# Performance work log

Hardware: AMD Instinct MI355X
Metric: run time of the kernel (lower is better)

The kernel has to match this reference:

```python
import jax, jax.numpy as jnp
import numpy as np

N_NODES = 100_000
N_EDGES = 3_200_000
D_FEAT = 128
L_FILTERS = 10  # filter_count_L
ALPHA = 0.3


def setup_inputs() -> dict:
    key = jax.random.key(0)
    k1, k2, k3, k4 = jax.random.split(key, 4)
    edge_row = jax.random.randint(k1, (N_EDGES,), 0, N_NODES, dtype=jnp.int32)
    edge_col = jax.random.randint(k2, (N_EDGES,), 0, N_NODES, dtype=jnp.int32)
    # scale ~1/avg_degree so the propagated signal stays well-conditioned over 10 hops
    edge_vals = jax.random.uniform(k3, (N_EDGES,), dtype=jnp.float32) * (1.0 / 32.0)
    X = jax.random.normal(k4, (N_NODES, D_FEAT), dtype=jnp.float32)
    # reset_parameters: gpr_weights[i] = alpha * (1-alpha)**i
    gpr_weights = ALPHA * (1.0 - ALPHA) ** jnp.arange(L_FILTERS + 1, dtype=jnp.float32)
    return {"edge_row": edge_row, "edge_col": edge_col, "edge_vals": edge_vals,
            "X": X, "gpr_weights": gpr_weights}


def reference(edge_row, edge_col, edge_vals, X, gpr_weights):
    """GPR filter bank: Z = sum_l w_l * A^l X (dropout is identity at inference)."""
    n = X.shape[0]
    H = X                                  # hop 0
    out = gpr_weights[0] * X
    for l in range(1, L_FILTERS + 1):
        msgs = edge_vals[:, None] * H[edge_col]          # [E, d] gather + scale
        H = jax.ops.segment_sum(msgs, edge_row, num_segments=n)  # SpMM row-scatter
        H = jnp.where(jnp.isfinite(H), H, jnp.zeros_like(H))     # non-finite guard
        out = out + gpr_weights[l] * H
    return out
```

## Files before the change

### kernel.cpp

```cpp
#include <hip/hip_runtime.h>
#include <math.h>

#define N_NODES   100000
#define D_FEAT    128
#define N_EDGES   3200000
#define L_FILTERS 10

#define RPB_LOG   7
#define RPB       128
#define NBUCKETS  ((N_NODES + RPB - 1) >> RPB_LOG)
#define CHUNK     8192
#define NA_BLOCKS ((N_EDGES + CHUNK - 1) / CHUNK)

typedef unsigned char  u8;
typedef unsigned int   u32;
typedef unsigned short u16;
typedef unsigned long long u64;
typedef float f32x2 __attribute__((ext_vector_type(2)));

static __device__ __forceinline__ u16 f2bf(float f) {
    u32 u = __float_as_uint(f);
    u32 r = (u + 0x7FFFu + ((u >> 16) & 1u)) >> 16;
    return (u16)r;
}
static __device__ __forceinline__ float bf2f(u32 b) {
    return __uint_as_float(b << 16);
}

__global__ void gpr_init(const float* __restrict__ X,
                         u16* __restrict__ Xbf, u8* __restrict__ Xf8, int n4) {
    int i = blockIdx.x * blockDim.x + threadIdx.x;
    if (i >= n4) return;
    float4 v = ((const float4*)X)[i];
    ushort4 b;
    b.x = f2bf(v.x); b.y = f2bf(v.y); b.z = f2bf(v.z); b.w = f2bf(v.w);
    ((ushort4*)Xbf)[i] = b;
    u32 p01 = __builtin_amdgcn_cvt_pk_fp8_f32(v.x, v.y, 0, false) & 0xFFFFu;
    u32 p23 = __builtin_amdgcn_cvt_pk_fp8_f32(v.z, v.w, 0, false) & 0xFFFFu;
    ((u32*)Xf8)[i] = p01 | (p23 << 16);
}

__global__ __launch_bounds__(256) void gpr_bucket_hist(const int* __restrict__ rows,
                                                       int* __restrict__ bcount) {
    __shared__ int hist[NBUCKETS];
    int t = threadIdx.x;
    for (int i = t; i < NBUCKETS; i += 256) hist[i] = 0;
    __syncthreads();
    int stride = gridDim.x * 256;
    for (int e = blockIdx.x * 256 + t; e < N_EDGES; e += stride)
        atomicAdd(&hist[rows[e] >> RPB_LOG], 1);
    __syncthreads();
    for (int i = t; i < NBUCKETS; i += 256)
        if (hist[i]) atomicAdd(&bcount[i], hist[i]);
}

__global__ __launch_bounds__(1024) void gpr_bucket_scan(const int* __restrict__ bcount,
                                                        int* __restrict__ bucket_base,
                                                        int* __restrict__ bucket_cursor,
                                                        int* __restrict__ row_ptr) {
    __shared__ int buf[1024];
    int t = threadIdx.x;
    int v = (t < NBUCKETS) ? bcount[t] : 0;
    buf[t] = v; __syncthreads();
    for (int off = 1; off < 1024; off <<= 1) {
        int x = (t >= off) ? buf[t - off] : 0;
        __syncthreads();
        buf[t] += x;
        __syncthreads();
    }
    if (t < NBUCKETS) {
        int ex = buf[t] - v;
        bucket_base[t] = ex;
        bucket_cursor[t] = ex;
    }
    if (t == 0) {
        bucket_base[NBUCKETS] = N_EDGES;
        row_ptr[N_NODES] = N_EDGES;
    }
}

__global__ __launch_bounds__(256) void gpr_binA(const int* __restrict__ rows,
                                                const int* __restrict__ cols,
                                                const float* __restrict__ vals,
                                                int* __restrict__ bucket_cursor,
                                                u64* __restrict__ packedA) {
    __shared__ u64 stage[CHUNK];
    __shared__ int hist[NBUCKETS];
    __shared__ int lbase[NBUCKETS];
    __shared__ int lcur[NBUCKETS];
    __shared__ int goff[NBUCKETS];
    __shared__ int psum[256];
    int t = threadIdx.x;
    long long base = (long long)blockIdx.x * CHUNK;
    for (int i = t; i < NBUCKETS; i += 256) hist[i] = 0;
    __syncthreads();
    for (int j = 0; j < CHUNK / 256; ++j) {
        long long e = base + j * 256 + t;
        if (e < N_EDGES) atomicAdd(&hist[rows[e] >> RPB_LOG], 1);
    }
    __syncthreads();
    int s = 0, b0 = t * 4;
    #pragma unroll
    for (int j = 0; j < 4; ++j) { int b = b0 + j; if (b < NBUCKETS) s += hist[b]; }
    psum[t] = s; __syncthreads();
    for (int off = 1; off < 256; off <<= 1) {
        int x = (t >= off) ? psum[t - off] : 0;
        __syncthreads();
        psum[t] += x;
        __syncthreads();
    }
    int run = psum[t] - s;
    #pragma unroll
    for (int j = 0; j < 4; ++j) {
        int b = b0 + j;
        if (b < NBUCKETS) { lbase[b] = run; run += hist[b]; }
    }
    __syncthreads();
    for (int i = t; i < NBUCKETS; i += 256) {
        lcur[i] = lbase[i];
        int g = (hist[i]) ? atomicAdd(&bucket_cursor[i], hist[i]) : 0;
        goff[i] = g - lbase[i];
    }
    __syncthreads();
    for (int j = 0; j < CHUNK / 256; ++j) {
        long long e = base + j * 256 + t;
        if (e < N_EDGES) {
            int r = rows[e];
            u32 vb = (u32)f2bf(vals[e]);
            u64 p = ((u64)vb << 34) | ((u64)(u32)r << 17) | (u64)(u32)cols[e];
            int pos = atomicAdd(&lcur[r >> RPB_LOG], 1);
            stage[pos] = p;
        }
    }
    __syncthreads();
    long long rem = (long long)N_EDGES - base;
    int total = (rem < CHUNK) ? (int)rem : CHUNK;
    for (int idx = t; idx < total; idx += 256) {
        u64 p = stage[idx];
        int b = (int)((p >> 17) & 0x1FFFFu) >> RPB_LOG;
        packedA[goff[b] + idx] = p;
    }
}

__global__ __launch_bounds__(256) void gpr_binB(const int* __restrict__ bucket_base,
                                                const u64* __restrict__ packedA,
                                                int* __restrict__ row_ptr,
                                                u32* __restrict__ edges) {
    __shared__ int cnt[RPB];
    __shared__ int sbuf[RPB];
    __shared__ int cur[RPB];
    int b = blockIdx.x;
    int t = threadIdx.x;
    int r0 = b << RPB_LOG;
    int r1 = r0 + RPB; if (r1 > N_NODES) r1 = N_NODES;
    int lo = bucket_base[b], hi = bucket_base[b + 1];
    if (t < RPB) cnt[t] = 0;
    __syncthreads();
    for (int e = lo + t; e < hi; e += 256) {
        int r = (int)((packedA[e] >> 17) & 0x1FFFFu);
        atomicAdd(&cnt[r - r0], 1);
    }
    __syncthreads();
    if (t < RPB) sbuf[t] = cnt[t];
    __syncthreads();
    for (int off = 1; off < RPB; off <<= 1) {
        int x = (t < RPB && t >= off) ? sbuf[t - off] : 0;
        __syncthreads();
        if (t < RPB) sbuf[t] += x;
        __syncthreads();
    }
    if (t < RPB) {
        int ex = sbuf[t] - cnt[t];
        cur[t] = ex;
        if (r0 + t < r1) row_ptr[r0 + t] = lo + ex;
    }
    __syncthreads();
    for (int e = lo + t; e < hi; e += 256) {
        u64 p = packedA[e];
        int r = (int)((p >> 17) & 0x1FFFFu);
        int pos = lo + atomicAdd(&cur[r - r0], 1);
        edges[pos] = (u32)(((p >> 34) << 17) | (p & 0x1FFFFu));
    }
}


#define IS8(EW, TT, H)                                                          \
    { _Pragma("unroll")                                                         \
      for (int j = 0; j < 8; ++j) {                                             \
          u32 es = (u32)__builtin_amdgcn_readlane((int)(EW), (TT) + j);         \
          H[j] = *(const u16*)((const u8*)H8 + (size_t)((es & 0x1FFFFu) << 7) + lane2); \
      } }

#define CO8(EW, M, TT, H, PX, PY)                                               \
    { _Pragma("unroll")                                                         \
      for (int j = 0; j < 8; ++j) {                                             \
          int t = (TT) + j;                                                     \
          u32 es = (u32)__builtin_amdgcn_readlane((int)(EW), t);                \
          float v = (t < (M)) ? __uint_as_float((es >> 17) << 16) : 0.0f;       \
          f32x2 f = __builtin_amdgcn_cvt_pk_f32_fp8(H[j], false);               \
          PX[j & 3] = fmaf(v, f[0], PX[j & 3]);                                 \
          PY[j & 3] = fmaf(v, f[1], PY[j & 3]);                                 \
      } }

#define PIPE(EW, M, PX, PY)                                                     \
    {                                                                           \
        u32 hA[8], hB[8];                                                       \
        IS8(EW, 0, hA)                                                          \
        if ((M) > 8)  IS8(EW, 8, hB)                                            \
        CO8(EW, M, 0, hA, PX, PY)                                               \
        if ((M) > 16) IS8(EW, 16, hA)                                           \
        if ((M) > 8)  CO8(EW, M, 8, hB, PX, PY)                                 \
        if ((M) > 24) IS8(EW, 24, hB)                                           \
        if ((M) > 16) CO8(EW, M, 16, hA, PX, PY)                                \
        if ((M) > 32) IS8(EW, 32, hA)                                           \
        if ((M) > 24) CO8(EW, M, 24, hB, PX, PY)                                \
        if ((M) > 40) IS8(EW, 40, hB)                                           \
        if ((M) > 32) CO8(EW, M, 32, hA, PX, PY)                                \
        if ((M) > 48) IS8(EW, 48, hA)                                           \
        if ((M) > 40) CO8(EW, M, 40, hB, PX, PY)                                \
        if ((M) > 56) IS8(EW, 56, hB)                                           \
        if ((M) > 48) CO8(EW, M, 48, hA, PX, PY)                                \
        if ((M) > 56) CO8(EW, M, 56, hB, PX, PY)                                \
    }

template<int WR>
__global__ __launch_bounds__(256) void gpr_spmm(
    const int* __restrict__ row_ptr, const u32* __restrict__ edges,
    const void* __restrict__ Zold, const u16* __restrict__ Xbf,
    const float* __restrict__ Xf, const float* __restrict__ w, int l,
    void* __restrict__ Znew, float* __restrict__ out) {
    int pr = (int)(blockIdx.x * 4 + (threadIdx.x >> 6));
    pr = __builtin_amdgcn_readfirstlane(pr);
    if (pr >= N_NODES / 2) return;
    int row0 = pr * 2;
    int lane = threadIdx.x & 63;
    int lane2 = lane * 2;
    int s0 = __builtin_amdgcn_readfirstlane(row_ptr[row0]);
    int e0 = __builtin_amdgcn_readfirstlane(row_ptr[row0 + 1]);
    int e1 = __builtin_amdgcn_readfirstlane(row_ptr[row0 + 2]);
    int len0 = e0 - s0, len1 = e1 - e0;
    int m0 = (len0 < 64) ? len0 : 64;
    int m1 = (len1 < 64) ? len1 : 64;

    const u16* H8 = (const u16*)Zold;

    u32 ew0 = 0, ew1 = 0;
    if (m0 > 0) { int tc = (lane < m0) ? lane : (m0 - 1); ew0 = edges[s0 + tc]; }
    if (m1 > 0) { int tc = (lane < m1) ? lane : (m1 - 1); ew1 = edges[e0 + tc]; }

    float ax[4] = {0.f,0.f,0.f,0.f}, ay[4] = {0.f,0.f,0.f,0.f};
    float bx[4] = {0.f,0.f,0.f,0.f}, by[4] = {0.f,0.f,0.f,0.f};

    PIPE(ew0, m0, ax, ay)
    for (int t0 = 64; t0 < len0; t0 += 64) {
        int rem = len0 - t0;
        int m = (rem < 64) ? rem : 64;
        int tc = (lane < m) ? lane : (m - 1);
        u32 ew = edges[s0 + t0 + tc];
        PIPE(ew, m, ax, ay)
    }
    PIPE(ew1, m1, bx, by)
    for (int t0 = 64; t0 < len1; t0 += 64) {
        int rem = len1 - t0;
        int m = (rem < 64) ? rem : 64;
        int tc = (lane < m) ? lane : (m - 1);
        u32 ew = edges[e0 + t0 + tc];
        PIPE(ew, m, bx, by)
    }

    float axs = (ax[0] + ax[1]) + (ax[2] + ax[3]);
    float ays = (ay[0] + ay[1]) + (ay[2] + ay[3]);
    float bxs = (bx[0] + bx[1]) + (bx[2] + bx[3]);
    float bys = (by[0] + by[1]) + (by[2] + by[3]);
    if (!isfinite(axs)) axs = 0.0f;
    if (!isfinite(ays)) ays = 0.0f;
    if (!isfinite(bxs)) bxs = 0.0f;
    if (!isfinite(bys)) bys = 0.0f;

    size_t o0 = (size_t)row0 * 64 + lane;
    size_t o1 = o0 + 64;
    if (WR == 2) {
        float w0 = w[0], w1 = w[1];
        float2 xv0 = ((const float2*)Xf)[o0];
        float2 xv1 = ((const float2*)Xf)[o1];
        f32x2 r0, r1;
        r0[0] = fmaf(w1, axs, w0 * xv0.x);
        r0[1] = fmaf(w1, ays, w0 * xv0.y);
        r1[0] = fmaf(w1, bxs, w0 * xv1.x);
        r1[1] = fmaf(w1, bys, w0 * xv1.y);
        __builtin_nontemporal_store(r0, &((f32x2*)out)[o0]);
        __builtin_nontemporal_store(r1, &((f32x2*)out)[o1]);
    } else {
        float cc = w[l + 1] / w[l];
        u32 xb0 = __builtin_nontemporal_load((const u32*)Xbf + o0);
        u32 xb1 = __builtin_nontemporal_load((const u32*)Xbf + o1);
        float z0x = fmaf(cc, axs, bf2f(xb0 & 0xFFFFu));
        float z0y = fmaf(cc, ays, bf2f(xb0 >> 16));
        float z1x = fmaf(cc, bxs, bf2f(xb1 & 0xFFFFu));
        float z1y = fmaf(cc, bys, bf2f(xb1 >> 16));
        u32 p0 = __builtin_amdgcn_cvt_pk_fp8_f32(z0x, z0y, 0, false);
        u32 p1 = __builtin_amdgcn_cvt_pk_fp8_f32(z1x, z1y, 0, false);
        __builtin_nontemporal_store((u16)p0, (u16*)Znew + o0);
        __builtin_nontemporal_store((u16)p1, (u16*)Znew + o1);
    }
}

extern "C" void kernel_launch(void* const* d_in, const int* in_sizes, int n_in,
                              void* d_out, int out_size, void* d_ws, size_t ws_size,
                              hipStream_t stream) {
    const int*   erow  = (const int*)d_in[0];
    const int*   ecol  = (const int*)d_in[1];
    const float* evals = (const float*)d_in[2];
    const float* X     = (const float*)d_in[3];
    const float* w     = (const float*)d_in[4];
    float* out = (float*)d_out;

    const size_t n = (size_t)N_NODES * D_FEAT;

    char* base = (char*)d_ws;
    u8*  Za      = (u8*)base;
    u8*  Zb      = (u8*)(base + n);
    u16* Xbf     = (u16*)(base + 2 * n);
    u64* packedA = (u64*)(base + 4 * n);
    int* row_ptr = (int*)(base + 6 * n);
    int* bucket_base   = row_ptr + 100352;
    int* bucket_cursor = bucket_base + 1024;
    int* bcount        = bucket_cursor + 1024;
    u32* edges   = (u32*)(bcount + 1024);

    dim3 b256(256);

    hipMemsetAsync(bcount, 0, NBUCKETS * sizeof(int), stream);
    gpr_bucket_hist<<<dim3(512), b256, 0, stream>>>(erow, bcount);
    gpr_bucket_scan<<<dim3(1), dim3(1024), 0, stream>>>(bcount, bucket_base, bucket_cursor, row_ptr);
    gpr_binA<<<dim3(NA_BLOCKS), b256, 0, stream>>>(erow, ecol, evals, bucket_cursor, packedA);
    gpr_binB<<<dim3(NBUCKETS), b256, 0, stream>>>(bucket_base, packedA, row_ptr, edges);

    gpr_init<<<dim3((unsigned)((n / 4 + 255) / 256)), b256, 0, stream>>>(X, Xbf, Za, (int)(n / 4));

    dim3 spmm_grid((N_NODES / 2 + 3) / 4);
    const void* Zold = Za;
    for (int k = L_FILTERS - 1; k >= 1; --k) {
        void* Znew = (Zold == (void*)Za) ? (void*)Zb : (void*)Za;
        gpr_spmm<0><<<spmm_grid, b256, 0, stream>>>(row_ptr, edges, Zold, Xbf, X, w, k, Znew, nullptr);
        Zold = Znew;
    }
    gpr_spmm<2><<<spmm_grid, b256, 0, stream>>>(row_ptr, edges, Zold, Xbf, X, w, 0, nullptr, out);
}
```

Baseline: 911.4 us.

## Store edges as 64-bit pre-shifted offset/value pairs and simplify the gather loop

The row-binning kernel now stages each bucket in LDS and writes its CSR edges back into packedA in place. Each edge is stored as a 64-bit word: a pre-shifted byte offset in the low half and fp32 value bits in the high half, which removes the separate u32 edge array. The SpMM inner loop reads the offset and value through two readlanes with no unpacking arithmetic. The hand-interleaved IS8/CO8 load pipeline is replaced by a plain loop over groups of eight plus a tail. The trade-offs are double the edge index traffic, 64 KB of LDS per block in the binning kernel, and losing the explicit overlap of gather loads with FMAs.

```diff
diff --git a/kernel.cpp b/kernel.cpp
--- a/kernel.cpp
+++ b/kernel.cpp
@@ -143,9 +143,9 @@
 }
 
 __global__ __launch_bounds__(256) void gpr_binB(const int* __restrict__ bucket_base,
-                                                const u64* __restrict__ packedA,
-                                                int* __restrict__ row_ptr,
-                                                u32* __restrict__ edges) {
+                                                u64* __restrict__ packedA,
+                                                int* __restrict__ row_ptr) {
+    __shared__ u64 stage[CHUNK];
     __shared__ int cnt[RPB];
     __shared__ int sbuf[RPB];
     __shared__ int cur[RPB];
@@ -154,11 +154,13 @@
     int r0 = b << RPB_LOG;
     int r1 = r0 + RPB; if (r1 > N_NODES) r1 = N_NODES;
     int lo = bucket_base[b], hi = bucket_base[b + 1];
+    int num = hi - lo;
     if (t < RPB) cnt[t] = 0;
     __syncthreads();
-    for (int e = lo + t; e < hi; e += 256) {
-        int r = (int)((packedA[e] >> 17) & 0x1FFFFu);
-        atomicAdd(&cnt[r - r0], 1);
+    for (int i = t; i < num; i += 256) {
+        u64 p = packedA[lo + i];
+        stage[i] = p;
+        atomicAdd(&cnt[((int)(p >> 17) & 0x1FFFF) - r0], 1);
     }
     __syncthreads();
     if (t < RPB) sbuf[t] = cnt[t];
@@ -175,57 +177,54 @@
         if (r0 + t < r1) row_ptr[r0 + t] = lo + ex;
     }
     __syncthreads();
-    for (int e = lo + t; e < hi; e += 256) {
-        u64 p = packedA[e];
+    for (int i = t; i < num; i += 256) {
+        u64 p = stage[i];
         int r = (int)((p >> 17) & 0x1FFFFu);
         int pos = lo + atomicAdd(&cur[r - r0], 1);
-        edges[pos] = (u32)(((p >> 34) << 17) | (p & 0x1FFFFu));
-    }
-}
-
-
-#define IS8(EW, TT, H)                                                          \
-    { _Pragma("unroll")                                                         \
-      for (int j = 0; j < 8; ++j) {                                             \
-          u32 es = (u32)__builtin_amdgcn_readlane((int)(EW), (TT) + j);         \
-          H[j] = *(const u16*)((const u8*)H8 + (size_t)((es & 0x1FFFFu) << 7) + lane2); \
-      } }
-
-#define CO8(EW, M, TT, H, PX, PY)                                               \
+        u32 vb  = (u32)(p >> 34);
+        u32 col = (u32)(p & 0x1FFFFu);
+        packedA[pos] = ((u64)(vb << 16) << 32) | (u64)(col << 7);
+    }
+}
+
+
+#define FULL8(EWLO, EWHI, TT, PX, PY)                                           \
     { _Pragma("unroll")                                                         \
       for (int j = 0; j < 8; ++j) {                                             \
           int t = (TT) + j;                                                     \
-          u32 es = (u32)__builtin_amdgcn_readlane((int)(EW), t);                \
-          float v = (t < (M)) ? __uint_as_float((es >> 17) << 16) : 0.0f;       \
-          f32x2 f = __builtin_amdgcn_cvt_pk_f32_fp8(H[j], false);               \
+          u32 off = (u32)__builtin_amdgcn_readlane((int)(EWLO), t);             \
+          u32 vh  = (u32)__builtin_amdgcn_readlane((int)(EWHI), t);             \
+          float v = __uint_as_float(vh);                                        \
+          u32 h = *(const u16*)(H8 + off + lane2);                              \
+          f32x2 f = __builtin_amdgcn_cvt_pk_f32_fp8(h, false);                  \
           PX[j & 3] = fmaf(v, f[0], PX[j & 3]);                                 \
           PY[j & 3] = fmaf(v, f[1], PY[j & 3]);                                 \
       } }
 
-#define PIPE(EW, M, PX, PY)                                                     \
+#define TAIL8(EWLO, EWHI, M, TT, PX, PY)                                        \
+    { _Pragma("unroll")                                                         \
+      for (int j = 0; j < 8; ++j) {                                             \
+          int t = (TT) + j;                                                     \
+          int tc = (t < (M)) ? t : ((M) - 1);                                   \
+          u32 off = (u32)__builtin_amdgcn_readlane((int)(EWLO), tc);            \
+          u32 vh  = (u32)__builtin_amdgcn_readlane((int)(EWHI), tc);            \
+          float v = (t < (M)) ? __uint_as_float(vh) : 0.0f;                     \
+          u32 h = *(const u16*)(H8 + off + lane2);                              \
+          f32x2 f = __builtin_amdgcn_cvt_pk_f32_fp8(h, false);                  \
+          PX[j & 3] = fmaf(v, f[0], PX[j & 3]);                                 \
+          PY[j & 3] = fmaf(v, f[1], PY[j & 3]);                                 \
+      } }
+
+#define PROC(EWLO, EWHI, M, PX, PY)                                             \
     {                                                                           \
-        u32 hA[8], hB[8];                                                       \
-        IS8(EW, 0, hA)                                                          \
-        if ((M) > 8)  IS8(EW, 8, hB)                                            \
-        CO8(EW, M, 0, hA, PX, PY)                                               \
-        if ((M) > 16) IS8(EW, 16, hA)                                           \
-        if ((M) > 8)  CO8(EW, M, 8, hB, PX, PY)                                 \
-        if ((M) > 24) IS8(EW, 24, hB)                                           \
-        if ((M) > 16) CO8(EW, M, 16, hA, PX, PY)                                \
-        if ((M) > 32) IS8(EW, 32, hA)                                           \
-        if ((M) > 24) CO8(EW, M, 24, hB, PX, PY)                                \
-        if ((M) > 40) IS8(EW, 40, hB)                                           \
-        if ((M) > 32) CO8(EW, M, 32, hA, PX, PY)                                \
-        if ((M) > 48) IS8(EW, 48, hA)                                           \
-        if ((M) > 40) CO8(EW, M, 40, hB, PX, PY)                                \
-        if ((M) > 56) IS8(EW, 56, hB)                                           \
-        if ((M) > 48) CO8(EW, M, 48, hA, PX, PY)                                \
-        if ((M) > 56) CO8(EW, M, 56, hB, PX, PY)                                \
+        int nfull = (M) & ~7;                                                   \
+        for (int tt = 0; tt < nfull; tt += 8) FULL8(EWLO, EWHI, tt, PX, PY)     \
+        if (nfull < (M)) TAIL8(EWLO, EWHI, M, nfull, PX, PY)                    \
     }
 
 template<int WR>
 __global__ __launch_bounds__(256) void gpr_spmm(
-    const int* __restrict__ row_ptr, const u32* __restrict__ edges,
+    const int* __restrict__ row_ptr, const u64* __restrict__ edges,
     const void* __restrict__ Zold, const u16* __restrict__ Xbf,
     const float* __restrict__ Xf, const float* __restrict__ w, int l,
     void* __restrict__ Znew, float* __restrict__ out) {
@@ -242,30 +241,40 @@
     int m0 = (len0 < 64) ? len0 : 64;
     int m1 = (len1 < 64) ? len1 : 64;
 
-    const u16* H8 = (const u16*)Zold;
-
-    u32 ew0 = 0, ew1 = 0;
-    if (m0 > 0) { int tc = (lane < m0) ? lane : (m0 - 1); ew0 = edges[s0 + tc]; }
-    if (m1 > 0) { int tc = (lane < m1) ? lane : (m1 - 1); ew1 = edges[e0 + tc]; }
+    const u8* H8 = (const u8*)Zold;
+
+    u32 ew0lo = 0, ew0hi = 0, ew1lo = 0, ew1hi = 0;
+    if (m0 > 0) {
+        int tc = (lane < m0) ? lane : (m0 - 1);
+        u64 ew = edges[s0 + tc];
+        ew0lo = (u32)ew; ew0hi = (u32)(ew >> 32);
+    }
+    if (m1 > 0) {
+        int tc = (lane < m1) ? lane : (m1 - 1);
+        u64 ew = edges[e0 + tc];
+        ew1lo = (u32)ew; ew1hi = (u32)(ew >> 32);
+    }
 
     float ax[4] = {0.f,0.f,0.f,0.f}, ay[4] = {0.f,0.f,0.f,0.f};
     float bx[4] = {0.f,0.f,0.f,0.f}, by[4] = {0.f,0.f,0.f,0.f};
 
-    PIPE(ew0, m0, ax, ay)
+    PROC(ew0lo, ew0hi, m0, ax, ay)
     for (int t0 = 64; t0 < len0; t0 += 64) {
         int rem = len0 - t0;
         int m = (rem < 64) ? rem : 64;
         int tc = (lane < m) ? lane : (m - 1);
-        u32 ew = edges[s0 + t0 + tc];
-        PIPE(ew, m, ax, ay)
-    }
-    PIPE(ew1, m1, bx, by)
+        u64 ew = edges[s0 + t0 + tc];
+        u32 elo = (u32)ew, ehi = (u32)(ew >> 32);
+        PROC(elo, ehi, m, ax, ay)
+    }
+    PROC(ew1lo, ew1hi, m1, bx, by)
     for (int t0 = 64; t0 < len1; t0 += 64) {
         int rem = len1 - t0;
         int m = (rem < 64) ? rem : 64;
         int tc = (lane < m) ? lane : (m - 1);
-        u32 ew = edges[e0 + t0 + tc];
-        PIPE(ew, m, bx, by)
+        u64 ew = edges[e0 + t0 + tc];
+        u32 elo = (u32)ew, ehi = (u32)(ew >> 32);
+        PROC(elo, ehi, m, bx, by)
     }
 
     float axs = (ax[0] + ax[1]) + (ax[2] + ax[3]);
@@ -326,7 +335,6 @@
     int* bucket_base   = row_ptr + 100352;
     int* bucket_cursor = bucket_base + 1024;
     int* bcount        = bucket_cursor + 1024;
-    u32* edges   = (u32*)(bcount + 1024);
 
     dim3 b256(256);
 
@@ -334,7 +342,7 @@
     gpr_bucket_hist<<<dim3(512), b256, 0, stream>>>(erow, bcount);
     gpr_bucket_scan<<<dim3(1), dim3(1024), 0, stream>>>(bcount, bucket_base, bucket_cursor, row_ptr);
     gpr_binA<<<dim3(NA_BLOCKS), b256, 0, stream>>>(erow, ecol, evals, bucket_cursor, packedA);
-    gpr_binB<<<dim3(NBUCKETS), b256, 0, stream>>>(bucket_base, packedA, row_ptr, edges);
+    gpr_binB<<<dim3(NBUCKETS), b256, 0, stream>>>(bucket_base, packedA, row_ptr);
 
     gpr_init<<<dim3((unsigned)((n / 4 + 255) / 256)), b256, 0, stream>>>(X, Xbf, Za, (int)(n / 4));
 
@@ -342,8 +350,8 @@
     const void* Zold = Za;
     for (int k = L_FILTERS - 1; k >= 1; --k) {
         void* Znew = (Zold == (void*)Za) ? (void*)Zb : (void*)Za;
-        gpr_spmm<0><<<spmm_grid, b256, 0, stream>>>(row_ptr, edges, Zold, Xbf, X, w, k, Znew, nullptr);
+        gpr_spmm<0><<<spmm_grid, b256, 0, stream>>>(row_ptr, packedA, Zold, Xbf, X, w, k, Znew, nullptr);
         Zold = Znew;
     }
-    gpr_spmm<2><<<spmm_grid, b256, 0, stream>>>(row_ptr, edges, Zold, Xbf, X, w, 0, nullptr, out);
-}
+    gpr_spmm<2><<<spmm_grid, b256, 0, stream>>>(row_ptr, packedA, Zold, Xbf, X, w, 0, nullptr, out);
+}
```

Result: no change. 900.9 us (-1.1%).
